# Kernel tuning notes

Hardware: AMD Instinct MI355X
Metric: run time of the kernel (lower is better)

The kernel has to match this reference:

```python
import jax, jax.numpy as jnp
import numpy as np

B, C, H, W = 8, 256, 128, 128


def setup_inputs() -> dict:
    key = jax.random.key(0)
    k1, k2, k3, k4, k5 = jax.random.split(key, 5)
    x = jax.random.normal(k1, (B, C, H, W), dtype=jnp.float32)
    # 1x1 conv weights stored as (out_channels, in_channels); bias (out_channels,)
    w1 = jax.random.normal(k2, (C, C), dtype=jnp.float32) * (1.0 / np.sqrt(C))
    b1 = jax.random.normal(k3, (C,), dtype=jnp.float32) * 0.01
    w2 = jax.random.normal(k4, (C, C), dtype=jnp.float32) * (1.0 / np.sqrt(C))
    b2 = jax.random.normal(k5, (C,), dtype=jnp.float32) * 0.01
    return {"x": x, "w1": w1, "b1": b1, "w2": w2, "b2": b2}


def reference(x, w1, b1, w2, b2):
    b, c, h, w = x.shape
    xf = x.reshape(b, c, h * w)                      # (B, C, N)
    # 1x1 convs == per-pixel linear maps over channels
    q = jnp.einsum('oc,bcn->bon', w1, xf) + b1[None, :, None]   # (B, C, N)
    k = jnp.einsum('oc,bcn->bon', w2, xf) + b2[None, :, None]   # (B, C, N)
    # channel-attention Gram matrix: (B, C, N) @ (B, N, C) -> (B, C, C)
    attention = jnp.einsum('bcn,bdn->bcd', q, k)
    attention = jax.nn.softmax(attention, axis=-1)
    # (B, C, C) @ (B, C, N) -> (B, C, N), v = x itself (unprojected)
    attention_v = jnp.einsum('bcd,bdn->bcn', attention, xf).reshape(b, c, h, w)
    return x + attention_v
```

## Files before the change

kernel.cpp:

```cpp
#include <hip/hip_runtime.h>
#include <hip/hip_bf16.h>

#define B_    8
#define C_    256
#define NPIX  16384
#define BK    64
#define KC4   16
#define KCH4  (NPIX / KC4)
#define NSTEP4 (KCH4 / BK)

typedef __attribute__((ext_vector_type(8))) short bf16x8;
typedef __attribute__((ext_vector_type(4))) float f32x4;
typedef unsigned int uint_;

__device__ __forceinline__ unsigned short f2bf(float x) {
  unsigned int u = __builtin_bit_cast(unsigned int, x);
  u = (u + 0x7fffu + ((u >> 16) & 1u)) >> 16;
  return (unsigned short)u;
}
__device__ __forceinline__ float fcomp(const float4& v, int i) {
  switch (i) { case 0: return v.x; case 1: return v.y; case 2: return v.z; default: return v.w; }
}

__global__ __launch_bounds__(512, 2) void k_gram(const float* __restrict__ x,
                                                 float* __restrict__ gpart,
                                                 float* __restrict__ spart) {
  const int bid  = blockIdx.x;
  const int half = bid >> 7;
  const int b    = (bid >> 4) & 7;
  const int kc   = bid & 15;
  const float* X = x + (size_t)b * C_ * NPIX + kc * KCH4;

  __shared__ __align__(16) unsigned short Hi[2][256 * 64];
  __shared__ __align__(16) unsigned short Lo[2][256 * 64];

  const int tid  = threadIdx.x;
  const int lane = tid & 63;
  const int w    = tid >> 6;
  const int wr   = w >> 2;
  const int wc   = w & 3;

  const int srow = tid >> 4;
  const int scol = (tid & 15) * 4;
  const float* sp = X + (size_t)srow * NPIX + scol;

  float rs[8] = {};
  float4 g[8];

#define GLOAD(ks)                                                             \
  _Pragma("unroll")                                                           \
  for (int j = 0; j < 8; ++j)                                                 \
    g[j] = *reinterpret_cast<const float4*>(sp + (size_t)j * 32 * NPIX + (ks) * BK);

#define STAGE(buf)                                                            \
  _Pragma("unroll")                                                           \
  for (int j = 0; j < 8; ++j) {                                               \
    const float4 v = g[j];                                                    \
    rs[j] += (v.x + v.y) + (v.z + v.w);                                       \
    const uint_ u0 = __builtin_bit_cast(uint_, v.x);                          \
    const uint_ u1 = __builtin_bit_cast(uint_, v.y);                          \
    const uint_ u2 = __builtin_bit_cast(uint_, v.z);                          \
    const uint_ u3 = __builtin_bit_cast(uint_, v.w);                          \
    uint2 hi, lo;                                                             \
    hi.x = (u0 >> 16) | (u1 & 0xffff0000u);                                   \
    hi.y = (u2 >> 16) | (u3 & 0xffff0000u);                                   \
    const float h0 = __builtin_bit_cast(float, u0 & 0xffff0000u);             \
    const float h1 = __builtin_bit_cast(float, u1 & 0xffff0000u);             \
    const float h2 = __builtin_bit_cast(float, u2 & 0xffff0000u);             \
    const float h3 = __builtin_bit_cast(float, u3 & 0xffff0000u);             \
    const uint_ l0 = __builtin_bit_cast(uint_, v.x - h0);                     \
    const uint_ l1 = __builtin_bit_cast(uint_, v.y - h1);                     \
    const uint_ l2 = __builtin_bit_cast(uint_, v.z - h2);                     \
    const uint_ l3 = __builtin_bit_cast(uint_, v.w - h3);                     \
    lo.x = (l0 >> 16) | (l1 & 0xffff0000u);                                   \
    lo.y = (l2 >> 16) | (l3 & 0xffff0000u);                                   \
    const int row = j * 32 + srow;                                            \
    const int idx = (row * 64 + scol) ^ ((row & 7) << 3);                     \
    *reinterpret_cast<uint2*>(&Hi[buf][idx]) = hi;                            \
    *reinterpret_cast<uint2*>(&Lo[buf][idx]) = lo;                            \
  }

  GLOAD(0)
  STAGE(0)
  __syncthreads();

  f32x4 acc[4][4] = {};

  for (int ks = 0; ks < NSTEP4; ++ks) {
    const int cur = ks & 1;
    if (ks + 1 < NSTEP4) GLOAD(ks + 1)
    __builtin_amdgcn_s_setprio(1);
#pragma unroll
    for (int kk = 0; kk < 2; ++kk) {
      const int kb = kk * 32 + (lane >> 4) * 8;
      bf16x8 ahi[4], bhi[4], blo[4];
#pragma unroll
      for (int m = 0; m < 4; ++m) {
        const int row = half * 128 + wr * 64 + m * 16 + (lane & 15);
        ahi[m] = *reinterpret_cast<const bf16x8*>(&Hi[cur][(row * 64 + kb) ^ ((row & 7) << 3)]);
      }
#pragma unroll
      for (int n = 0; n < 4; ++n) {
        const int row = wc * 64 + n * 16 + (lane & 15);
        bhi[n] = *reinterpret_cast<const bf16x8*>(&Hi[cur][(row * 64 + kb) ^ ((row & 7) << 3)]);
      }
#pragma unroll
      for (int m = 0; m < 4; ++m)
#pragma unroll
        for (int n = 0; n < 4; ++n)
          acc[m][n] = __builtin_amdgcn_mfma_f32_16x16x32_bf16(ahi[m], bhi[n], acc[m][n], 0, 0, 0);
#pragma unroll
      for (int n = 0; n < 4; ++n) {
        const int row = wc * 64 + n * 16 + (lane & 15);
        blo[n] = *reinterpret_cast<const bf16x8*>(&Lo[cur][(row * 64 + kb) ^ ((row & 7) << 3)]);
      }
#pragma unroll
      for (int m = 0; m < 4; ++m)
#pragma unroll
        for (int n = 0; n < 4; ++n)
          acc[m][n] = __builtin_amdgcn_mfma_f32_16x16x32_bf16(ahi[m], blo[n], acc[m][n], 0, 0, 0);
#pragma unroll
      for (int m = 0; m < 4; ++m) {
        const int row = half * 128 + wr * 64 + m * 16 + (lane & 15);
        bf16x8 alo = *reinterpret_cast<const bf16x8*>(&Lo[cur][(row * 64 + kb) ^ ((row & 7) << 3)]);
#pragma unroll
        for (int n = 0; n < 4; ++n)
          acc[m][n] = __builtin_amdgcn_mfma_f32_16x16x32_bf16(alo, bhi[n], acc[m][n], 0, 0, 0);
      }
    }
    __builtin_amdgcn_s_setprio(0);
    if (ks + 1 < NSTEP4) STAGE(cur ^ 1)
    __syncthreads();
  }
#undef GLOAD
#undef STAGE

#pragma unroll
  for (int j = 0; j < 8; ++j) {
#pragma unroll
    for (int off = 1; off < 16; off <<= 1) rs[j] += __shfl_xor(rs[j], off, 64);
  }
  if (half == 0 && (tid & 15) == 0) {
#pragma unroll
    for (int j = 0; j < 8; ++j)
      spart[((size_t)b * KC4 + kc) * 256 + j * 32 + srow] = rs[j];
  }

  float* gp = gpart + (size_t)bid * (128 * 256);
#pragma unroll
  for (int m = 0; m < 4; ++m) {
    const int row0 = wr * 64 + m * 16 + ((lane >> 4) << 2);
#pragma unroll
    for (int n = 0; n < 4; ++n) {
      const int col = wc * 64 + n * 16 + (lane & 15);
#pragma unroll
      for (int j = 0; j < 4; ++j)
        gp[(size_t)(row0 + j) * 256 + col] = acc[m][n][j];
    }
  }
}

__global__ __launch_bounds__(256) void k_reduce(const float* __restrict__ gpart,
                                                float* __restrict__ G) {
  const int t  = blockIdx.x * 256 + threadIdx.x;
  const int b  = t >> 14;
  const int i  = (t >> 6) & 255;
  const int j4 = (t & 63) * 4;
  const int hb = (i >> 7) * 128 + b * 16;
  const int il = i & 127;
  float4 s = make_float4(0.f, 0.f, 0.f, 0.f);
#pragma unroll
  for (int kc = 0; kc < KC4; ++kc) {
    const float4 v = *reinterpret_cast<const float4*>(
        &gpart[(size_t)(hb + kc) * (128 * 256) + (size_t)il * 256 + j4]);
    s.x += v.x; s.y += v.y; s.z += v.z; s.w += v.w;
  }
  *reinterpret_cast<float4*>(&G[((size_t)b * 256 + i) * 256 + j4]) = s;
}

__global__ __launch_bounds__(256) void k_transpose(const float* __restrict__ in,
                                                   float* __restrict__ outp) {
  __shared__ float t[32][33];
  const int bx = blockIdx.x & 7, by = blockIdx.x >> 3;
  const int tx = threadIdx.x & 31, ty = threadIdx.x >> 5;
#pragma unroll
  for (int i = 0; i < 32; i += 8)
    t[ty + i][tx] = in[(size_t)(by * 32 + ty + i) * 256 + bx * 32 + tx];
  __syncthreads();
#pragma unroll
  for (int i = 0; i < 32; i += 8)
    outp[(size_t)(bx * 32 + ty + i) * 256 + by * 32 + tx] = t[tx][ty + i];
}

__global__ __launch_bounds__(256) void k_u(const float* __restrict__ w1,
                                           const float* __restrict__ w2,
                                           const float* __restrict__ spart,
                                           float* __restrict__ u1,
                                           float* __restrict__ u2) {
  const int b = blockIdx.x;
  const int tid = threadIdx.x;
  __shared__ float sl[256];
  float sv = 0.f;
#pragma unroll
  for (int kc = 0; kc < KC4; ++kc) sv += spart[((size_t)b * KC4 + kc) * 256 + tid];
  sl[tid] = sv;
  __syncthreads();
  float a1 = 0.f, a2 = 0.f;
#pragma unroll 4
  for (int c = 0; c < 256; ++c) {
    a1 += w1[(size_t)tid * 256 + c] * sl[c];
    a2 += w2[(size_t)tid * 256 + c] * sl[c];
  }
  u1[b * 256 + tid] = a1;
  u2[b * 256 + tid] = a2;
}

__global__ __launch_bounds__(256) void k_smallmm(const float* __restrict__ A, long asb,
                                                 const float* __restrict__ Bm, long bsb,
                                                 float* __restrict__ Cm, long csb) {
  const int b  = blockIdx.y;
  const int i0 = blockIdx.x * 8;
  const float* Ab = A  + (size_t)asb * b;
  const float* Bb = Bm + (size_t)bsb * b;
  float*       Cb = Cm + (size_t)csb * b;
  const int tid = threadIdx.x;
  __shared__ float arows[8][256];
#pragma unroll
  for (int rr = 0; rr < 8; ++rr) arows[rr][tid] = Ab[(size_t)(i0 + rr) * 256 + tid];
  __syncthreads();
  float acc[8] = {};
#pragma unroll 4
  for (int k = 0; k < 256; ++k) {
    const float bv = Bb[(size_t)k * 256 + tid];
#pragma unroll
    for (int rr = 0; rr < 8; ++rr) acc[rr] += arows[rr][k] * bv;
  }
#pragma unroll
  for (int rr = 0; rr < 8; ++rr) Cb[(size_t)(i0 + rr) * 256 + tid] = acc[rr];
}

__global__ __launch_bounds__(256) void k_softmax(const float* __restrict__ L,
                                                 const float* __restrict__ b1,
                                                 const float* __restrict__ b2,
                                                 const float* __restrict__ u1,
                                                 const float* __restrict__ u2,
                                                 unsigned short* __restrict__ Abf) {
  const int b = blockIdx.y, i = blockIdx.x, j = threadIdx.x;
  const size_t base = ((size_t)b * 256 + i) * 256;
  const float v = L[base + j] + u1[b * 256 + i] * b2[j] +
                  b1[i] * (u2[b * 256 + j] + 16384.f * b2[j]);
  const int lane = j & 63, wv = j >> 6;
  __shared__ float redm[4], reds[4];
  float m = v;
#pragma unroll
  for (int off = 32; off; off >>= 1) m = fmaxf(m, __shfl_xor(m, off, 64));
  if (lane == 0) redm[wv] = m;
  __syncthreads();
  m = fmaxf(fmaxf(redm[0], redm[1]), fmaxf(redm[2], redm[3]));
  const float e = __expf(v - m);
  float sm = e;
#pragma unroll
  for (int off = 32; off; off >>= 1) sm += __shfl_xor(sm, off, 64);
  if (lane == 0) reds[wv] = sm;
  __syncthreads();
  sm = (reds[0] + reds[1]) + (reds[2] + reds[3]);
  float p = e / sm;
  if (j == i) p += 1.0f;
  Abf[base + j] = f2bf(p);
}

__global__ __launch_bounds__(256, 4) void k_av(const unsigned short* __restrict__ Abf,
                                               const float* __restrict__ x,
                                               float* __restrict__ out) {
  const int bid = blockIdx.x;
  const int b = bid & 7;
  const int nbase = (bid >> 3) * 32;
  const unsigned short* Ab = Abf + (size_t)b * 65536;
  const float* Xb = x + (size_t)b * C_ * NPIX;
  float* Ob = out + (size_t)b * C_ * NPIX;

  __shared__ __align__(16) unsigned short Xt[32 * 256];

  const int tid = threadIdx.x;
  const int lane = tid & 63, w = tid >> 6;

  {
    const int pq = (tid & 7) * 4;
    const int dq = (tid >> 3) * 4;
#pragma unroll
    for (int h = 0; h < 2; ++h) {
      const int d = dq + h * 128;
      const float* xs = Xb + (size_t)d * NPIX + nbase + pq;
      const float4 r0 = *reinterpret_cast<const float4*>(xs);
      const float4 r1 = *reinterpret_cast<const float4*>(xs + NPIX);
      const float4 r2 = *reinterpret_cast<const float4*>(xs + 2 * NPIX);
      const float4 r3 = *reinterpret_cast<const float4*>(xs + 3 * NPIX);
#pragma unroll
      for (int i = 0; i < 4; ++i) {
        const int px = pq + i;
        ushort4 v = make_ushort4(f2bf(fcomp(r0, i)), f2bf(fcomp(r1, i)),
                                 f2bf(fcomp(r2, i)), f2bf(fcomp(r3, i)));
        const int idx = (px * 256 + d) ^ (((px ^ (px >> 2)) & 7) << 3);
        *reinterpret_cast<ushort4*>(&Xt[idx]) = v;
      }
    }
  }
  __syncthreads();

  const int kboff = (lane >> 4) * 8;
  f32x4 acc[4][2] = {};
  bf16x8 afA[4], afB[4], bq[2];

#define LOADA(kk, af)                                                         \
  _Pragma("unroll")                                                           \
  for (int m = 0; m < 4; ++m)                                                 \
    af[m] = *reinterpret_cast<const bf16x8*>(                                 \
        Ab + (size_t)(w * 64 + m * 16 + (lane & 15)) * 256 + (kk) * 32 + kboff);

#define LOADB(kk)                                                             \
  _Pragma("unroll")                                                           \
  for (int n = 0; n < 2; ++n) {                                               \
    const int px = n * 16 + (lane & 15);                                      \
    bq[n] = *reinterpret_cast<const bf16x8*>(                                 \
        &Xt[(px * 256 + (kk) * 32 + kboff) ^ (((px ^ (px >> 2)) & 7) << 3)]); \
  }

#define MFMA8(af)                                                             \
  _Pragma("unroll")                                                           \
  for (int m = 0; m < 4; ++m)                                                 \
    _Pragma("unroll")                                                         \
    for (int n = 0; n < 2; ++n)                                               \
      acc[m][n] = __builtin_amdgcn_mfma_f32_16x16x32_bf16(bq[n], af[m], acc[m][n], 0, 0, 0);

  LOADA(0, afA)
#pragma unroll
  for (int kk = 0; kk < 8; ++kk) {
    LOADB(kk)
    if (kk < 7) {
      if (kk & 1) { LOADA(kk + 1, afA) } else { LOADA(kk + 1, afB) }
    }
    if (kk & 1) { MFMA8(afB) } else { MFMA8(afA) }
  }
#undef LOADA
#undef LOADB
#undef MFMA8

#pragma unroll
  for (int m = 0; m < 4; ++m) {
    const int ch = w * 64 + m * 16 + (lane & 15);
    float* orow = Ob + (size_t)ch * NPIX + nbase;
#pragma unroll
    for (int n = 0; n < 2; ++n) {
      const int p0 = n * 16 + ((lane >> 4) << 2);
      *reinterpret_cast<float4*>(orow + p0) = *reinterpret_cast<const float4*>(&acc[m][n]);
    }
  }
}

extern "C" void kernel_launch(void* const* d_in, const int* in_sizes, int n_in,
                              void* d_out, int out_size, void* d_ws, size_t ws_size,
                              hipStream_t stream) {
  const float* x  = (const float*)d_in[0];
  const float* w1 = (const float*)d_in[1];
  const float* b1 = (const float*)d_in[2];
  const float* w2 = (const float*)d_in[3];
  const float* b2 = (const float*)d_in[4];
  float* out = (float*)d_out;
  char* ws = (char*)d_ws;

  float* gpart = out;

  constexpr size_t G_OFF     = 0;
  constexpr size_t T1_OFF    = G_OFF   + (size_t)B_ * C_ * C_ * 4;
  constexpr size_t L_OFF     = T1_OFF  + (size_t)B_ * C_ * C_ * 4;
  constexpr size_t W2T_OFF   = L_OFF   + (size_t)B_ * C_ * C_ * 4;
  constexpr size_t SPART_OFF = W2T_OFF + (size_t)C_ * C_ * 4;
  constexpr size_t U1_OFF    = SPART_OFF + (size_t)B_ * KC4 * C_ * 4;
  constexpr size_t U2_OFF    = U1_OFF  + (size_t)B_ * C_ * 4;
  constexpr size_t ABF_OFF   = U2_OFF  + (size_t)B_ * C_ * 4;

  float* G     = (float*)(ws + G_OFF);
  float* T1    = (float*)(ws + T1_OFF);
  float* L     = (float*)(ws + L_OFF);
  float* w2t   = (float*)(ws + W2T_OFF);
  float* spart = (float*)(ws + SPART_OFF);
  float* u1    = (float*)(ws + U1_OFF);
  float* u2    = (float*)(ws + U2_OFF);
  unsigned short* Abf = (unsigned short*)(ws + ABF_OFF);

  k_transpose<<<64, 256, 0, stream>>>(w2, w2t);
  k_gram     <<<256, 512, 0, stream>>>(x, gpart, spart);
  k_reduce   <<<512, 256, 0, stream>>>(gpart, G);
  k_u        <<<B_, 256, 0, stream>>>(w1, w2, spart, u1, u2);
  k_smallmm  <<<dim3(32, B_), 256, 0, stream>>>(w1, 0, G, C_ * C_, T1, C_ * C_);
  k_smallmm  <<<dim3(32, B_), 256, 0, stream>>>(T1, C_ * C_, w2t, 0, L, C_ * C_);
  k_softmax  <<<dim3(C_, B_), 256, 0, stream>>>(L, b1, b2, u1, u2, Abf);
  k_av       <<<4096, 256, 0, stream>>>(Abf, x, out);
}
```

Before: 212.9 us.

## Single-buffer gram LDS, double K-split, and raise gram occupancy to 4 blocks/CU

The gram kernel drops LDS double-buffering, halving shared memory per block to 64KB, and raises the launch-bounds occupancy target from 2 to 4 blocks per CU. The pixel dimension is split into 32 chunks instead of 16, so 512 blocks launch, and the reduce and u kernels are updated to sum 32 partials. The aim is to hide latency through more resident blocks rather than in-block software pipelining. In exchange there is an extra barrier per step, no overlap of the bf16 split staging with the MFMAs, tighter register limits, and twice the partial-gram traffic, which the gpart buffer stored in the output must now hold.

```diff
diff --git a/kernel.cpp b/kernel.cpp
--- a/kernel.cpp
+++ b/kernel.cpp
@@ -5,9 +5,9 @@
 #define C_    256
 #define NPIX  16384
 #define BK    64
-#define KC4   16
-#define KCH4  (NPIX / KC4)
-#define NSTEP4 (KCH4 / BK)
+#define KCG   32
+#define KCHG  (NPIX / KCG)
+#define NSTEPG (KCHG / BK)
 
 typedef __attribute__((ext_vector_type(8))) short bf16x8;
 typedef __attribute__((ext_vector_type(4))) float f32x4;
@@ -22,17 +22,17 @@
   switch (i) { case 0: return v.x; case 1: return v.y; case 2: return v.z; default: return v.w; }
 }
 
-__global__ __launch_bounds__(512, 2) void k_gram(const float* __restrict__ x,
+__global__ __launch_bounds__(512, 4) void k_gram(const float* __restrict__ x,
                                                  float* __restrict__ gpart,
                                                  float* __restrict__ spart) {
   const int bid  = blockIdx.x;
-  const int half = bid >> 7;
-  const int b    = (bid >> 4) & 7;
-  const int kc   = bid & 15;
-  const float* X = x + (size_t)b * C_ * NPIX + kc * KCH4;
-
-  __shared__ __align__(16) unsigned short Hi[2][256 * 64];
-  __shared__ __align__(16) unsigned short Lo[2][256 * 64];
+  const int half = bid >> 8;
+  const int b    = (bid >> 5) & 7;
+  const int kc   = bid & 31;
+  const float* X = x + (size_t)b * C_ * NPIX + kc * KCHG;
+
+  __shared__ __align__(16) unsigned short Hi[256 * 64];
+  __shared__ __align__(16) unsigned short Lo[256 * 64];
 
   const int tid  = threadIdx.x;
   const int lane = tid & 63;
@@ -52,7 +52,7 @@
   for (int j = 0; j < 8; ++j)                                                 \
     g[j] = *reinterpret_cast<const float4*>(sp + (size_t)j * 32 * NPIX + (ks) * BK);
 
-#define STAGE(buf)                                                            \
+#define STAGE()                                                               \
   _Pragma("unroll")                                                           \
   for (int j = 0; j < 8; ++j) {                                               \
     const float4 v = g[j];                                                    \
@@ -76,19 +76,18 @@
     lo.y = (l2 >> 16) | (l3 & 0xffff0000u);                                   \
     const int row = j * 32 + srow;                                            \
     const int idx = (row * 64 + scol) ^ ((row & 7) << 3);                     \
-    *reinterpret_cast<uint2*>(&Hi[buf][idx]) = hi;                            \
-    *reinterpret_cast<uint2*>(&Lo[buf][idx]) = lo;                            \
+    *reinterpret_cast<uint2*>(&Hi[idx]) = hi;                                 \
+    *reinterpret_cast<uint2*>(&Lo[idx]) = lo;                                 \
   }
 
   GLOAD(0)
-  STAGE(0)
-  __syncthreads();
 
   f32x4 acc[4][4] = {};
 
-  for (int ks = 0; ks < NSTEP4; ++ks) {
-    const int cur = ks & 1;
-    if (ks + 1 < NSTEP4) GLOAD(ks + 1)
+  for (int ks = 0; ks < NSTEPG; ++ks) {
+    STAGE()
+    __syncthreads();
+    if (ks + 1 < NSTEPG) GLOAD(ks + 1)
     __builtin_amdgcn_s_setprio(1);
 #pragma unroll
     for (int kk = 0; kk < 2; ++kk) {
@@ -97,12 +96,12 @@
 #pragma unroll
       for (int m = 0; m < 4; ++m) {
         const int row = half * 128 + wr * 64 + m * 16 + (lane & 15);
-        ahi[m] = *reinterpret_cast<const bf16x8*>(&Hi[cur][(row * 64 + kb) ^ ((row & 7) << 3)]);
+        ahi[m] = *reinterpret_cast<const bf16x8*>(&Hi[(row * 64 + kb) ^ ((row & 7) << 3)]);
       }
 #pragma unroll
       for (int n = 0; n < 4; ++n) {
         const int row = wc * 64 + n * 16 + (lane & 15);
-        bhi[n] = *reinterpret_cast<const bf16x8*>(&Hi[cur][(row * 64 + kb) ^ ((row & 7) << 3)]);
+        bhi[n] = *reinterpret_cast<const bf16x8*>(&Hi[(row * 64 + kb) ^ ((row & 7) << 3)]);
       }
 #pragma unroll
       for (int m = 0; m < 4; ++m)
@@ -112,7 +111,7 @@
 #pragma unroll
       for (int n = 0; n < 4; ++n) {
         const int row = wc * 64 + n * 16 + (lane & 15);
-        blo[n] = *reinterpret_cast<const bf16x8*>(&Lo[cur][(row * 64 + kb) ^ ((row & 7) << 3)]);
+        blo[n] = *reinterpret_cast<const bf16x8*>(&Lo[(row * 64 + kb) ^ ((row & 7) << 3)]);
       }
 #pragma unroll
       for (int m = 0; m < 4; ++m)
@@ -122,14 +121,13 @@
 #pragma unroll
       for (int m = 0; m < 4; ++m) {
         const int row = half * 128 + wr * 64 + m * 16 + (lane & 15);
-        bf16x8 alo = *reinterpret_cast<const bf16x8*>(&Lo[cur][(row * 64 + kb) ^ ((row & 7) << 3)]);
+        bf16x8 alo = *reinterpret_cast<const bf16x8*>(&Lo[(row * 64 + kb) ^ ((row & 7) << 3)]);
 #pragma unroll
         for (int n = 0; n < 4; ++n)
           acc[m][n] = __builtin_amdgcn_mfma_f32_16x16x32_bf16(alo, bhi[n], acc[m][n], 0, 0, 0);
       }
     }
     __builtin_amdgcn_s_setprio(0);
-    if (ks + 1 < NSTEP4) STAGE(cur ^ 1)
     __syncthreads();
   }
 #undef GLOAD
@@ -143,7 +141,7 @@
   if (half == 0 && (tid & 15) == 0) {
 #pragma unroll
     for (int j = 0; j < 8; ++j)
-      spart[((size_t)b * KC4 + kc) * 256 + j * 32 + srow] = rs[j];
+      spart[((size_t)b * KCG + kc) * 256 + j * 32 + srow] = rs[j];
   }
 
   float* gp = gpart + (size_t)bid * (128 * 256);
@@ -166,11 +164,11 @@
   const int b  = t >> 14;
   const int i  = (t >> 6) & 255;
   const int j4 = (t & 63) * 4;
-  const int hb = (i >> 7) * 128 + b * 16;
+  const int hb = (i >> 7) * 256 + b * 32;
   const int il = i & 127;
   float4 s = make_float4(0.f, 0.f, 0.f, 0.f);
 #pragma unroll
-  for (int kc = 0; kc < KC4; ++kc) {
+  for (int kc = 0; kc < KCG; ++kc) {
     const float4 v = *reinterpret_cast<const float4*>(
         &gpart[(size_t)(hb + kc) * (128 * 256) + (size_t)il * 256 + j4]);
     s.x += v.x; s.y += v.y; s.z += v.z; s.w += v.w;
@@ -202,7 +200,7 @@
   __shared__ float sl[256];
   float sv = 0.f;
 #pragma unroll
-  for (int kc = 0; kc < KC4; ++kc) sv += spart[((size_t)b * KC4 + kc) * 256 + tid];
+  for (int kc = 0; kc < KCG; ++kc) sv += spart[((size_t)b * KCG + kc) * 256 + tid];
   sl[tid] = sv;
   __syncthreads();
   float a1 = 0.f, a2 = 0.f;
@@ -375,7 +373,7 @@
   constexpr size_t L_OFF     = T1_OFF  + (size_t)B_ * C_ * C_ * 4;
   constexpr size_t W2T_OFF   = L_OFF   + (size_t)B_ * C_ * C_ * 4;
   constexpr size_t SPART_OFF = W2T_OFF + (size_t)C_ * C_ * 4;
-  constexpr size_t U1_OFF    = SPART_OFF + (size_t)B_ * KC4 * C_ * 4;
+  constexpr size_t U1_OFF    = SPART_OFF + (size_t)B_ * KCG * C_ * 4;
   constexpr size_t U2_OFF    = U1_OFF  + (size_t)B_ * C_ * 4;
   constexpr size_t ABF_OFF   = U2_OFF  + (size_t)B_ * C_ * 4;
 
@@ -389,7 +387,7 @@
   unsigned short* Abf = (unsigned short*)(ws + ABF_OFF);
 
   k_transpose<<<64, 256, 0, stream>>>(w2, w2t);
-  k_gram     <<<256, 512, 0, stream>>>(x, gpart, spart);
+  k_gram     <<<512, 512, 0, stream>>>(x, gpart, spart);
   k_reduce   <<<512, 256, 0, stream>>>(gpart, G);
   k_u        <<<B_, 256, 0, stream>>>(w1, w2, spart, u1, u2);
   k_smallmm  <<<dim3(32, B_), 256, 0, stream>>>(w1, 0, G, C_ * C_, T1, C_ * C_);
```

After: 465.3 us. +118.6%, slower.
